# Kernel tuning notes

Measured on AMD Instinct MI355X. Metric: run time of the kernel, lower is better.

The kernel has to match this reference:

```python
import jax, jax.numpy as jnp
import numpy as np

N = 32768      # nodes
E = 1048576    # edges (avg degree 32)
H = 64         # hidden dim
T = 5          # message-passing rounds

def _mlp(x, W1, b1, W2, b2):
    # two-layer MLP with ReLU, applied row-wise
    return jax.nn.relu(x @ W1 + b1) @ W2 + b2

def setup_inputs() -> dict:
    key = jax.random.key(0)
    ks = jax.random.split(key, 24)
    g = lambda i, shape: jax.random.normal(ks[i], shape, dtype=jnp.float32) * (1.0 / np.sqrt(shape[0]))
    inp = {
        "nodes": jax.random.normal(ks[0], (N,), dtype=jnp.float32),
        "edges_init": jax.random.normal(ks[1], (E,), dtype=jnp.float32),
        "receivers": jax.random.randint(ks[2], (E,), 0, N, dtype=jnp.int32),
        "senders": jax.random.randint(ks[3], (E,), 0, N, dtype=jnp.int32),
        # NodeEncoder: 1 -> H -> H
        "Wne1": g(4, (1, H)), "bne1": jnp.zeros((H,), jnp.float32),
        "Wne2": g(5, (H, H)), "bne2": jnp.zeros((H,), jnp.float32),
        # EdgeEncoder: 1 -> H -> H
        "Wee1": g(6, (1, H)), "bee1": jnp.zeros((H,), jnp.float32),
        "Wee2": g(7, (H, H)), "bee2": jnp.zeros((H,), jnp.float32),
        # MessagePass edge-update MLP: [e, n_s, n_r] (3H) -> H -> H
        "Weu1": g(8, (3 * H, H)), "beu1": jnp.zeros((H,), jnp.float32),
        "Weu2": g(9, (H, H)), "beu2": jnp.zeros((H,), jnp.float32),
        # MessagePass node-update MLP: [n, agg] (2H) -> H -> H
        "Wnu1": g(10, (2 * H, H)), "bnu1": jnp.zeros((H,), jnp.float32),
        "Wnu2": g(11, (H, H)), "bnu2": jnp.zeros((H,), jnp.float32),
        # EdgeDecoder: H -> H -> 1
        "Wd1": g(12, (H, H)), "bd1": jnp.zeros((H,), jnp.float32),
        "Wd2": g(13, (H, 1)), "bd2": jnp.zeros((1,), jnp.float32),
        "alpha": jnp.float32(0.1),
    }
    return inp

def reference(nodes, edges_init, receivers, senders,
              Wne1, bne1, Wne2, bne2,
              Wee1, bee1, Wee2, bee2,
              Weu1, beu1, Weu2, beu2,
              Wnu1, bnu1, Wnu2, bnu2,
              Wd1, bd1, Wd2, bd2, alpha):
    norm = jnp.abs(edges_init).max()
    e = (edges_init / norm)[:, None]                   # [E,1]
    n = _mlp(nodes[:, None], Wne1, bne1, Wne2, bne2)   # [N,H]
    e = _mlp(e, Wee1, bee1, Wee2, bee2)                # [E,H]
    for _ in range(T):
        m = jnp.concatenate([e, n[senders], n[receivers]], axis=-1)  # [E,3H]
        e = _mlp(m, Weu1, beu1, Weu2, beu2)                          # [E,H]
        agg = jax.ops.segment_sum(e, receivers, num_segments=N)     # [N,H]
        n = _mlp(jnp.concatenate([n, agg], axis=-1), Wnu1, bnu1, Wnu2, bnu2)
    d = _mlp(e, Wd1, bd1, Wd2, bd2)[:, 0]              # [E]
    edges = edges_init + alpha * (d * norm)
    # graph_tril: keep lower-triangular entries (row=receiver >= col=sender);
    # sparse lower-tri matrix = BCOO((edges, [receivers, senders])); we return its values.
    edges = jnp.where(receivers >= senders, edges, jnp.float32(0.0))
    return edges
```

## Files before the change

kernel.cpp:

```cpp
#include <hip/hip_runtime.h>

#define NN 32768
#define NE 1048576
#define BCAP 5120

typedef __bf16 bf16_t;
typedef __bf16 bf16x8 __attribute__((ext_vector_type(8)));
typedef __bf16 bf16x4 __attribute__((ext_vector_type(4)));
typedef float f32x4 __attribute__((ext_vector_type(4)));
typedef unsigned int u32;
typedef unsigned short u16;

__global__ __launch_bounds__(256) void prep_encode_kernel(
    const float* __restrict__ Weu1, const float* __restrict__ Weu2,
    const float* __restrict__ Wee2, const float* __restrict__ Wd1,
    const float* __restrict__ Wnu1, const float* __restrict__ Wnu2,
    bf16_t* __restrict__ wfr,
    const float* __restrict__ nodes, const float* __restrict__ Wne1,
    const float* __restrict__ bne1, const float* __restrict__ Wne2,
    const float* __restrict__ bne2, bf16_t* __restrict__ n_bf) {
  const int b = blockIdx.x, tid = threadIdx.x;
  if (b < 144) {
    int idx = b * 256 + tid;
    int i = idx & 7, lane = (idx >> 3) & 63, f = idx >> 9;
    const float* W;
    int fl;
    if (f < 24)      { W = Weu1; fl = f; }
    else if (f < 32) { W = Weu2; fl = f - 24; }
    else if (f < 40) { W = Wee2; fl = f - 32; }
    else if (f < 48) { W = Wd1;  fl = f - 40; }
    else if (f < 64) { W = Wnu1; fl = f - 48; }
    else             { W = Wnu2; fl = f - 64; }
    int kt = fl >> 2, nt = fl & 3;
    int k = kt * 32 + ((lane >> 4) << 3) + i;
    int col = nt * 16 + (lane & 15);
    wfr[idx] = (bf16_t)W[k * 64 + col];
  } else {
    __shared__ float hs[4][64];
    int wid = tid >> 6, k = tid & 63;
    int node = (b - 144) * 4 + wid;
    float x = nodes[node];
    hs[wid][k] = fmaxf(x * Wne1[k] + bne1[k], 0.0f);
    __syncthreads();
    float acc = bne2[k];
#pragma unroll 8
    for (int j = 0; j < 64; ++j) acc = fmaf(hs[wid][j], Wne2[j * 64 + k], acc);
    n_bf[(size_t)node * 64 + k] = (bf16_t)acc;
  }
}

__global__ __launch_bounds__(256) void coarse_kernel(
    const float* __restrict__ edges_init, const int* __restrict__ recv,
    float* __restrict__ norm, u32* __restrict__ ccur,
    u16* __restrict__ bkt_r, u32* __restrict__ bkt_o) {
  __shared__ u32 hist[256];
  __shared__ u32 base[256];
  __shared__ float mred[4];
  const int tid = threadIdx.x, lane = tid & 63, wid = tid >> 6;
  const int idx = blockIdx.x * 256 + tid;
  hist[tid] = 0;
  __syncthreads();
  int4 r = reinterpret_cast<const int4*>(recv)[idx];
  float4 v = reinterpret_cast<const float4*>(edges_init)[idx];
  float m = fmaxf(fmaxf(fabsf(v.x), fabsf(v.y)), fmaxf(fabsf(v.z), fabsf(v.w)));
#pragma unroll
  for (int off = 32; off > 0; off >>= 1) m = fmaxf(m, __shfl_xor(m, off, 64));
  if (lane == 0) mred[wid] = m;
  atomicAdd(&hist[r.x >> 7], 1u);
  atomicAdd(&hist[r.y >> 7], 1u);
  atomicAdd(&hist[r.z >> 7], 1u);
  atomicAdd(&hist[r.w >> 7], 1u);
  __syncthreads();
  if (tid == 0) {
    float mm = fmaxf(fmaxf(mred[0], mred[1]), fmaxf(mred[2], mred[3]));
    atomicMax(reinterpret_cast<u32*>(norm), __float_as_uint(mm));
  }
  u32 h = hist[tid];
  if (h) base[tid] = atomicAdd(&ccur[tid], h);
  hist[tid] = 0;
  __syncthreads();
  const int e0 = idx * 4;
  int rv4[4] = {r.x, r.y, r.z, r.w};
#pragma unroll
  for (int q = 0; q < 4; ++q) {
    int rv = rv4[q], bk = rv >> 7;
    u32 loc = atomicAdd(&hist[bk], 1u);
    u32 pos = (u32)bk * BCAP + base[bk] + loc;
    bkt_r[pos] = (u16)rv;
    bkt_o[pos] = (u32)(e0 + q);
  }
}

__global__ __launch_bounds__(256) void scan256_kernel(const u32* __restrict__ ccur,
                                                      u32* __restrict__ bbase,
                                                      int* __restrict__ row_ptr) {
  __shared__ u32 s[256];
  const int tid = threadIdx.x;
  s[tid] = ccur[tid];
  __syncthreads();
  if (tid == 0) {
    u32 run = 0;
    for (int j = 0; j < 256; ++j) {
      u32 c = s[j];
      s[j] = run;
      run += c;
    }
    row_ptr[NN] = (int)run;
  }
  __syncthreads();
  bbase[tid] = s[tid];
}

__global__ __launch_bounds__(1024) void bucket_kernel(
    const u32* __restrict__ ccur, const u32* __restrict__ bbase,
    const u16* __restrict__ bkt_r, const u32* __restrict__ bkt_o,
    const int* __restrict__ senders, const float* __restrict__ edges_init,
    int* __restrict__ row_ptr, int* __restrict__ col_idx,
    int* __restrict__ s_perm, int* __restrict__ r_perm, float* __restrict__ x_perm) {
  __shared__ u32 hist[128];
  __shared__ u32 cur[128];
  const int b = blockIdx.x, tid = threadIdx.x;
  const u32 sz = ccur[b], bb = bbase[b];
  if (tid < 128) hist[tid] = 0;
  __syncthreads();
  for (u32 i = tid; i < sz; i += 1024) atomicAdd(&hist[bkt_r[(u32)b * BCAP + i] & 127], 1u);
  __syncthreads();
  if (tid == 0) {
    u32 run = 0;
    for (int j = 0; j < 128; ++j) {
      u32 c = hist[j];
      hist[j] = run;
      cur[j] = run;
      run += c;
    }
  }
  __syncthreads();
  if (tid < 128) row_ptr[b * 128 + tid] = (int)(bb + hist[tid]);
  for (u32 i = tid; i < sz; i += 1024) {
    int rv = (int)bkt_r[(u32)b * BCAP + i];
    int o = (int)bkt_o[(u32)b * BCAP + i];
    u32 loc = atomicAdd(&cur[rv & 127], 1u);
    u32 pos = bb + loc;
    col_idx[pos] = o;
    s_perm[pos] = senders[o];
    r_perm[pos] = rv;
    x_perm[pos] = edges_init[o];
  }
}

template <int MODE>
__global__ __launch_bounds__(256) void edge_update_kernel(
    bf16_t* __restrict__ e, const bf16_t* __restrict__ n_bf,
    const int* __restrict__ col_idx,
    const int* __restrict__ s_perm, const int* __restrict__ r_perm,
    const float* __restrict__ x_perm,
    const bf16_t* __restrict__ wfr,
    const float* __restrict__ beu1, const float* __restrict__ beu2,
    const float* __restrict__ Wee1, const float* __restrict__ bee1,
    const float* __restrict__ bee2, const float* __restrict__ norm_p,
    const float* __restrict__ bd1, const float* __restrict__ Wd2,
    const float* __restrict__ bd2_p, const float* __restrict__ alpha_p,
    float* __restrict__ out) {
  __shared__ alignas(16) bf16_t wstage[40 * 512];
  __shared__ alignas(16) bf16_t tr[4][16][72];
  __shared__ alignas(16) float fconst[448];
  const int tid = threadIdx.x, lane = tid & 63, wid = tid >> 6;
  const int l15 = lane & 15, lg = lane >> 4;

#pragma unroll
  for (int j = 0; j < 10; ++j) {
    int c = j * 256 + tid;
    int slot = c >> 6, within = c & 63;
    int sf = (slot < 32) ? slot : (MODE == 2 ? slot + 8 : slot);
    *reinterpret_cast<bf16x8*>(wstage + slot * 512 + within * 8) =
        *reinterpret_cast<const bf16x8*>(wfr + (size_t)sf * 512 + within * 8);
  }
  for (int c = tid; c < 448; c += 256) {
    float v;
    if (c < 64)       v = Wee1[c];
    else if (c < 128) v = bee1[c - 64];
    else if (c < 192) v = bee2[c - 128];
    else if (c < 256) v = bd1[c - 192];
    else if (c < 320) v = Wd2[c - 256];
    else if (c < 384) v = beu1[c - 320];
    else              v = beu2[c - 384];
    fconst[c] = v;
  }
  __syncthreads();

  float invn = 0.f;
  if constexpr (MODE == 0) invn = 1.0f / *norm_p;
  float nrm = 0.f, alp = 0.f, b2s = 0.f;
  if constexpr (MODE == 2) { nrm = *norm_p; alp = *alpha_p; b2s = *bd2_p; }

  const int nb = gridDim.x, cpx = nb >> 3;
  const int bs = (blockIdx.x & 7) * cpx + (blockIdx.x >> 3);
  const int NWAVE = nb * 4;
  const int NG = NE / 16;
  const int g0 = bs * 4 + wid;

  int sA, rA, oA, sB, rB, oB, sC, rC, oC;
  float pxA = 0.f, pxB = 0.f, pxC = 0.f;
  bf16x8 eA0, eA1, eB0, eB1, eC0, eC1;
  bf16x8 nA0, nA1, nA2, nA3, nB0, nB1, nB2, nB3;

  auto P1 = [&](int g, int& s, int& r, int& o, float& px, bf16x8& e0, bf16x8& e1) {
    int row = g * 16 + l15;
    s = s_perm[row];
    r = r_perm[row];
    if constexpr (MODE != 1) px = x_perm[row];
    if constexpr (MODE == 2) o = col_idx[row];
    if constexpr (MODE != 0) {
      const bf16x8* er = reinterpret_cast<const bf16x8*>(e + (size_t)row * 64);
      e0 = er[lg];
      e1 = er[4 + lg];
    }
  };
  auto P2 = [&](int s, int r, bf16x8& n0, bf16x8& n1, bf16x8& n2, bf16x8& n3) {
    const bf16x8* sp = reinterpret_cast<const bf16x8*>(n_bf + (size_t)s * 64);
    n0 = sp[lg];
    n1 = sp[4 + lg];
    const bf16x8* rp = reinterpret_cast<const bf16x8*>(n_bf + (size_t)r * 64);
    n2 = rp[lg];
    n3 = rp[4 + lg];
  };

  if (g0 < NG) {
    P1(g0, sA, rA, oA, pxA, eA0, eA1);
    P2(sA, rA, nA0, nA1, nA2, nA3);
    int g1 = g0 + NWAVE;
    if (g1 < NG) P1(g1, sB, rB, oB, pxB, eB0, eB1);
  }

  for (int g = g0; g < NG; g += NWAVE) {
    const int gB = g + NWAVE, gC = g + 2 * NWAVE;
    if (gB < NG) P2(sB, rB, nB0, nB1, nB2, nB3);
    if (gC < NG) P1(gC, sC, rC, oC, pxC, eC0, eC1);

    bf16x8 ce0, ce1;
    if constexpr (MODE == 0) {
      float xv = pxA * invn;
      f32x4 wl0 = *reinterpret_cast<const f32x4*>(&fconst[lg * 8]);
      f32x4 wl1 = *reinterpret_cast<const f32x4*>(&fconst[lg * 8 + 4]);
      f32x4 wh0 = *reinterpret_cast<const f32x4*>(&fconst[32 + lg * 8]);
      f32x4 wh1 = *reinterpret_cast<const f32x4*>(&fconst[32 + lg * 8 + 4]);
      f32x4 bl0 = *reinterpret_cast<const f32x4*>(&fconst[64 + lg * 8]);
      f32x4 bl1 = *reinterpret_cast<const f32x4*>(&fconst[64 + lg * 8 + 4]);
      f32x4 bh0 = *reinterpret_cast<const f32x4*>(&fconst[96 + lg * 8]);
      f32x4 bh1 = *reinterpret_cast<const f32x4*>(&fconst[96 + lg * 8 + 4]);
      bf16x8 h0, h1;
#pragma unroll
      for (int i = 0; i < 4; ++i) {
        h0[i]     = (bf16_t)fmaxf(fmaf(xv, wl0[i], bl0[i]), 0.0f);
        h0[4 + i] = (bf16_t)fmaxf(fmaf(xv, wl1[i], bl1[i]), 0.0f);
        h1[i]     = (bf16_t)fmaxf(fmaf(xv, wh0[i], bh0[i]), 0.0f);
        h1[4 + i] = (bf16_t)fmaxf(fmaf(xv, wh1[i], bh1[i]), 0.0f);
      }
      f32x4 ae[4];
#pragma unroll
      for (int nt = 0; nt < 4; ++nt)
        ae[nt] = *reinterpret_cast<const f32x4*>(&fconst[128 + nt * 16 + lg * 4]);
#pragma unroll
      for (int kt = 0; kt < 2; ++kt)
#pragma unroll
        for (int nt = 0; nt < 4; ++nt) {
          bf16x8 wf = *reinterpret_cast<const bf16x8*>(wstage + (32 + kt * 4 + nt) * 512 + lane * 8);
          ae[nt] = __builtin_amdgcn_mfma_f32_16x16x32_bf16(wf, kt ? h1 : h0, ae[nt], 0, 0, 0);
        }
#pragma unroll
      for (int nt = 0; nt < 4; ++nt) {
        bf16x4 pk;
#pragma unroll
        for (int r = 0; r < 4; ++r) pk[r] = (bf16_t)ae[nt][r];
        *reinterpret_cast<bf16x4*>(&tr[wid][l15][nt * 16 + lg * 4]) = pk;
      }
      ce0 = *reinterpret_cast<const bf16x8*>(&tr[wid][l15][lg * 8]);
      ce1 = *reinterpret_cast<const bf16x8*>(&tr[wid][l15][32 + lg * 8]);
    } else {
      ce0 = eA0;
      ce1 = eA1;
    }

    f32x4 acc[4];
#pragma unroll
    for (int nt = 0; nt < 4; ++nt)
      acc[nt] = *reinterpret_cast<const f32x4*>(&fconst[320 + nt * 16 + lg * 4]);
#pragma unroll
    for (int kt = 0; kt < 6; ++kt) {
      bf16x8 m = (kt == 0) ? ce0 : (kt == 1) ? ce1 : (kt == 2) ? nA0
               : (kt == 3) ? nA1 : (kt == 4) ? nA2 : nA3;
#pragma unroll
      for (int nt = 0; nt < 4; ++nt) {
        bf16x8 w = *reinterpret_cast<const bf16x8*>(wstage + (kt * 4 + nt) * 512 + lane * 8);
        acc[nt] = __builtin_amdgcn_mfma_f32_16x16x32_bf16(w, m, acc[nt], 0, 0, 0);
      }
    }

#pragma unroll
    for (int nt = 0; nt < 4; ++nt) {
      bf16x4 pk;
#pragma unroll
      for (int r = 0; r < 4; ++r) pk[r] = (bf16_t)fmaxf(acc[nt][r], 0.0f);
      *reinterpret_cast<bf16x4*>(&tr[wid][l15][nt * 16 + lg * 4]) = pk;
    }
    bf16x8 hh0 = *reinterpret_cast<const bf16x8*>(&tr[wid][l15][lg * 8]);
    bf16x8 hh1 = *reinterpret_cast<const bf16x8*>(&tr[wid][l15][32 + lg * 8]);

    f32x4 acc2[4];
#pragma unroll
    for (int nt = 0; nt < 4; ++nt)
      acc2[nt] = *reinterpret_cast<const f32x4*>(&fconst[384 + nt * 16 + lg * 4]);
#pragma unroll
    for (int kt = 0; kt < 2; ++kt)
#pragma unroll
      for (int nt = 0; nt < 4; ++nt) {
        bf16x8 w = *reinterpret_cast<const bf16x8*>(wstage + (24 + kt * 4 + nt) * 512 + lane * 8);
        acc2[nt] = __builtin_amdgcn_mfma_f32_16x16x32_bf16(w, kt ? hh1 : hh0, acc2[nt], 0, 0, 0);
      }

    if constexpr (MODE == 2) {
#pragma unroll
      for (int nt = 0; nt < 4; ++nt) {
        bf16x4 pk;
#pragma unroll
        for (int r = 0; r < 4; ++r) pk[r] = (bf16_t)acc2[nt][r];
        *reinterpret_cast<bf16x4*>(&tr[wid][l15][nt * 16 + lg * 4]) = pk;
      }
      bf16x8 eb0 = *reinterpret_cast<const bf16x8*>(&tr[wid][l15][lg * 8]);
      bf16x8 eb1 = *reinterpret_cast<const bf16x8*>(&tr[wid][l15][32 + lg * 8]);
      f32x4 ad[4];
#pragma unroll
      for (int nt = 0; nt < 4; ++nt)
        ad[nt] = *reinterpret_cast<const f32x4*>(&fconst[192 + nt * 16 + lg * 4]);
#pragma unroll
      for (int kt = 0; kt < 2; ++kt)
#pragma unroll
        for (int nt = 0; nt < 4; ++nt) {
          bf16x8 wf = *reinterpret_cast<const bf16x8*>(wstage + (32 + kt * 4 + nt) * 512 + lane * 8);
          ad[nt] = __builtin_amdgcn_mfma_f32_16x16x32_bf16(wf, kt ? eb1 : eb0, ad[nt], 0, 0, 0);
        }
      float s = 0.0f;
#pragma unroll
      for (int nt = 0; nt < 4; ++nt) {
        f32x4 w2 = *reinterpret_cast<const f32x4*>(&fconst[256 + nt * 16 + lg * 4]);
#pragma unroll
        for (int r = 0; r < 4; ++r) s = fmaf(fmaxf(ad[nt][r], 0.0f), w2[r], s);
      }
      s += __shfl_xor(s, 16, 64);
      s += __shfl_xor(s, 32, 64);
      if (lg == 0) {
        float dv = s + b2s;
        out[oA] = (rA >= sA) ? fmaf(alp * nrm, dv, pxA) : 0.0f;
      }
    } else {
#pragma unroll
      for (int nt = 0; nt < 4; ++nt) {
        bf16x4 pk;
#pragma unroll
        for (int r = 0; r < 4; ++r) pk[r] = (bf16_t)acc2[nt][r];
        *reinterpret_cast<bf16x4*>(&tr[wid][l15][nt * 16 + lg * 4]) = pk;
      }
      const int rr = lane >> 3, cc = lane & 7;
      bf16x8 w0 = *reinterpret_cast<const bf16x8*>(&tr[wid][rr][cc * 8]);
      bf16x8 w1 = *reinterpret_cast<const bf16x8*>(&tr[wid][8 + rr][cc * 8]);
      *reinterpret_cast<bf16x8*>(e + (size_t)(g * 16 + rr) * 64 + cc * 8) = w0;
      *reinterpret_cast<bf16x8*>(e + (size_t)(g * 16 + 8 + rr) * 64 + cc * 8) = w1;
    }

    sA = sB; rA = rB; oA = oB; pxA = pxB;
    eA0 = eB0; eA1 = eB1;
    nA0 = nB0; nA1 = nB1; nA2 = nB2; nA3 = nB3;
    sB = sC; rB = rC; oB = oC; pxB = pxC;
    eB0 = eC0; eB1 = eC1;
  }
}

__global__ __launch_bounds__(256) void agg_kernel(const bf16_t* __restrict__ e,
                                                  const int* __restrict__ row_ptr,
                                                  bf16_t* __restrict__ agg) {
  const int lane = threadIdx.x & 63, wid = threadIdx.x >> 6;
  const int rsub = lane >> 3;
  const int gw = blockIdx.x * 4 + wid, NWV = gridDim.x * 4;
  for (int node = gw; node < NN; node += NWV) {
    const int p0 = row_ptr[node], cnt = row_ptr[node + 1] - p0;
    float a[8] = {0, 0, 0, 0, 0, 0, 0, 0};
    const bf16x8* bb = reinterpret_cast<const bf16x8*>(e + (size_t)p0 * 64) + lane;
    const int nchunk = (cnt + 7) >> 3;
    int c = 0;
    for (; c + 4 <= nchunk; c += 4) {
      bf16x8 v0 = bb[(size_t)(c + 0) * 64];
      bf16x8 v1 = bb[(size_t)(c + 1) * 64];
      bf16x8 v2 = bb[(size_t)(c + 2) * 64];
      bf16x8 v3 = bb[(size_t)(c + 3) * 64];
      {
#pragma unroll
        for (int i = 0; i < 8; ++i) a[i] += (float)v0[i];
#pragma unroll
        for (int i = 0; i < 8; ++i) a[i] += (float)v1[i];
#pragma unroll
        for (int i = 0; i < 8; ++i) a[i] += (float)v2[i];
      }
      if ((c + 3) * 8 + rsub < cnt) {
#pragma unroll
        for (int i = 0; i < 8; ++i) a[i] += (float)v3[i];
      }
    }
    for (; c < nchunk; ++c) {
      bf16x8 v = bb[(size_t)c * 64];
      if (c * 8 + rsub < cnt) {
#pragma unroll
        for (int i = 0; i < 8; ++i) a[i] += (float)v[i];
      }
    }
#pragma unroll
    for (int i = 0; i < 8; ++i) {
      a[i] += __shfl_xor(a[i], 8, 64);
      a[i] += __shfl_xor(a[i], 16, 64);
      a[i] += __shfl_xor(a[i], 32, 64);
    }
    if (lane < 8) {
      bf16x8 pk;
#pragma unroll
      for (int i = 0; i < 8; ++i) pk[i] = (bf16_t)a[i];
      *reinterpret_cast<bf16x8*>(agg + (size_t)node * 64 + lane * 8) = pk;
    }
  }
}

__global__ __launch_bounds__(256) void node_mlp_kernel(
    const bf16_t* __restrict__ agg, const bf16_t* __restrict__ wfr,
    const float* __restrict__ bnu1, const float* __restrict__ bnu2,
    bf16_t* __restrict__ n_bf) {
  __shared__ alignas(16) bf16_t w2s[8 * 512];
  __shared__ alignas(16) bf16_t xb[4][16][72];
  const int tid = threadIdx.x, lane = tid & 63, wid = tid >> 6;
  const int l15 = lane & 15, lg = lane >> 4;

  bf16x8 W1r[16];
#pragma unroll
  for (int f = 0; f < 16; ++f)
    W1r[f] = *reinterpret_cast<const bf16x8*>(wfr + (size_t)(48 + f) * 512 + lane * 8);
#pragma unroll
  for (int j = 0; j < 2; ++j)
    reinterpret_cast<bf16x8*>(w2s)[j * 256 + tid] =
        reinterpret_cast<const bf16x8*>(wfr + (size_t)64 * 512)[j * 256 + tid];
  __syncthreads();

  f32x4 b1q[4], b2q[4];
#pragma unroll
  for (int nt = 0; nt < 4; ++nt) {
    b1q[nt] = *reinterpret_cast<const f32x4*>(bnu1 + nt * 16 + lg * 4);
    b2q[nt] = *reinterpret_cast<const f32x4*>(bnu2 + nt * 16 + lg * 4);
  }

  const int NT = NN / 16;
  for (int task = blockIdx.x * 4 + wid; task < NT; task += gridDim.x * 4) {
    const int base = task * 16;
    bf16x8 xn0 = *reinterpret_cast<const bf16x8*>(n_bf + (size_t)(base + l15) * 64 + lg * 8);
    bf16x8 xn1 = *reinterpret_cast<const bf16x8*>(n_bf + (size_t)(base + l15) * 64 + 32 + lg * 8);
    bf16x8 xa0 = *reinterpret_cast<const bf16x8*>(agg + (size_t)(base + l15) * 64 + lg * 8);
    bf16x8 xa1 = *reinterpret_cast<const bf16x8*>(agg + (size_t)(base + l15) * 64 + 32 + lg * 8);
    f32x4 acc[4];
#pragma unroll
    for (int nt = 0; nt < 4; ++nt) acc[nt] = b1q[nt];
#pragma unroll
    for (int kt = 0; kt < 4; ++kt) {
      bf16x8 x = (kt == 0) ? xn0 : (kt == 1) ? xn1 : (kt == 2) ? xa0 : xa1;
#pragma unroll
      for (int nt = 0; nt < 4; ++nt)
        acc[nt] = __builtin_amdgcn_mfma_f32_16x16x32_bf16(W1r[kt * 4 + nt], x, acc[nt], 0, 0, 0);
    }
#pragma unroll
    for (int nt = 0; nt < 4; ++nt) {
      bf16x4 pk;
#pragma unroll
      for (int r = 0; r < 4; ++r) pk[r] = (bf16_t)fmaxf(acc[nt][r], 0.0f);
      *reinterpret_cast<bf16x4*>(&xb[wid][l15][nt * 16 + lg * 4]) = pk;
    }
    bf16x8 hh0 = *reinterpret_cast<const bf16x8*>(&xb[wid][l15][lg * 8]);
    bf16x8 hh1 = *reinterpret_cast<const bf16x8*>(&xb[wid][l15][32 + lg * 8]);
    f32x4 acc2[4];
#pragma unroll
    for (int nt = 0; nt < 4; ++nt) acc2[nt] = b2q[nt];
#pragma unroll
    for (int kt = 0; kt < 2; ++kt)
#pragma unroll
      for (int nt = 0; nt < 4; ++nt) {
        bf16x8 w = *reinterpret_cast<const bf16x8*>(w2s + (kt * 4 + nt) * 512 + lane * 8);
        acc2[nt] = __builtin_amdgcn_mfma_f32_16x16x32_bf16(w, kt ? hh1 : hh0, acc2[nt], 0, 0, 0);
      }
#pragma unroll
    for (int nt = 0; nt < 4; ++nt) {
      bf16x4 pk;
#pragma unroll
      for (int r = 0; r < 4; ++r) pk[r] = (bf16_t)acc2[nt][r];
      *reinterpret_cast<bf16x4*>(n_bf + (size_t)(base + l15) * 64 + nt * 16 + lg * 4) = pk;
    }
  }
}

extern "C" void kernel_launch(void* const* d_in, const int* in_sizes, int n_in,
                              void* d_out, int out_size, void* d_ws, size_t ws_size,
                              hipStream_t stream) {
  const float* nodes      = (const float*)d_in[0];
  const float* edges_init = (const float*)d_in[1];
  const int*   receivers  = (const int*)d_in[2];
  const int*   senders    = (const int*)d_in[3];
  const float* Wne1 = (const float*)d_in[4];
  const float* bne1 = (const float*)d_in[5];
  const float* Wne2 = (const float*)d_in[6];
  const float* bne2 = (const float*)d_in[7];
  const float* Wee1 = (const float*)d_in[8];
  const float* bee1 = (const float*)d_in[9];
  const float* Wee2 = (const float*)d_in[10];
  const float* bee2 = (const float*)d_in[11];
  const float* Weu1 = (const float*)d_in[12];
  const float* beu1 = (const float*)d_in[13];
  const float* Weu2 = (const float*)d_in[14];
  const float* beu2 = (const float*)d_in[15];
  const float* Wnu1 = (const float*)d_in[16];
  const float* bnu1 = (const float*)d_in[17];
  const float* Wnu2 = (const float*)d_in[18];
  const float* bnu2 = (const float*)d_in[19];
  const float* Wd1  = (const float*)d_in[20];
  const float* bd1  = (const float*)d_in[21];
  const float* Wd2  = (const float*)d_in[22];
  const float* bd2  = (const float*)d_in[23];
  const float* alpha = (const float*)d_in[24];
  float* out = (float*)d_out;
  (void)in_sizes; (void)n_in; (void)out_size; (void)ws_size;

  char* ws = (char*)d_ws;
  size_t off = 0;
  auto alloc = [&](size_t bytes) -> void* {
    void* p = ws + off;
    off = (off + bytes + 255) & ~(size_t)255;
    return p;
  };
  float*  norm    = (float*)alloc(4);
  u32*    ccur    = (u32*)alloc(sizeof(u32) * 256);
  u32*    bbase   = (u32*)alloc(sizeof(u32) * 256);
  int*    row_ptr = (int*)alloc(sizeof(int) * (NN + 1));
  u16*    bkt_r   = (u16*)alloc(sizeof(u16) * 256 * BCAP);
  u32*    bkt_o   = (u32*)alloc(sizeof(u32) * 256 * BCAP);
  int*    col_idx = (int*)alloc(sizeof(int) * NE);
  int*    s_perm  = (int*)alloc(sizeof(int) * NE);
  int*    r_perm  = (int*)alloc(sizeof(int) * NE);
  float*  x_perm  = (float*)alloc(sizeof(float) * NE);
  bf16_t* n_bf    = (bf16_t*)alloc(sizeof(bf16_t) * (size_t)NN * 64);
  bf16_t* agg     = (bf16_t*)alloc(sizeof(bf16_t) * (size_t)NN * 64);
  bf16_t* e_buf   = (bf16_t*)alloc(sizeof(bf16_t) * (size_t)NE * 64 + 4096);
  bf16_t* wfr     = (bf16_t*)alloc(sizeof(bf16_t) * 72 * 512);

  hipMemsetAsync(norm, 0, 4, stream);
  hipMemsetAsync(ccur, 0, sizeof(u32) * 256, stream);

  prep_encode_kernel<<<8336, 256, 0, stream>>>(Weu1, Weu2, Wee2, Wd1, Wnu1, Wnu2, wfr,
                                               nodes, Wne1, bne1, Wne2, bne2, n_bf);
  coarse_kernel<<<1024, 256, 0, stream>>>(edges_init, receivers, norm, ccur, bkt_r, bkt_o);
  scan256_kernel<<<1, 256, 0, stream>>>(ccur, bbase, row_ptr);
  bucket_kernel<<<256, 1024, 0, stream>>>(ccur, bbase, bkt_r, bkt_o, senders, edges_init,
                                          row_ptr, col_idx, s_perm, r_perm, x_perm);

  edge_update_kernel<0><<<768, 256, 0, stream>>>(
      e_buf, n_bf, col_idx, s_perm, r_perm, x_perm, wfr, beu1, beu2,
      Wee1, bee1, bee2, norm, bd1, Wd2, bd2, alpha, out);
  for (int t = 1; t <= 4; ++t) {
    agg_kernel<<<2048, 256, 0, stream>>>(e_buf, row_ptr, agg);
    node_mlp_kernel<<<512, 256, 0, stream>>>(agg, wfr, bnu1, bnu2, n_bf);
    if (t < 4)
      edge_update_kernel<1><<<768, 256, 0, stream>>>(
          e_buf, n_bf, col_idx, s_perm, r_perm, x_perm, wfr, beu1, beu2,
          Wee1, bee1, bee2, norm, bd1, Wd2, bd2, alpha, out);
    else
      edge_update_kernel<2><<<768, 256, 0, stream>>>(
          e_buf, n_bf, col_idx, s_perm, r_perm, x_perm, wfr, beu1, beu2,
          Wee1, bee1, bee2, norm, bd1, Wd2, bd2, alpha, out);
  }
}
```

Baseline: 606.2 us.

## Fuse segment aggregation with node MLP and raise priority around MFMA loops

Merges agg_kernel and node_mlp_kernel into one kernel. Each block aggregates 16 nodes into shared memory, then a single wave runs the two-layer node MLP on them. This removes one launch per round and the global agg buffer round trip. In exchange, three of four waves idle during the MLP, and every block reloads the weights into registers and LDS. It also wraps the MFMA loops in the edge update kernel with s_setprio so those waves get issue priority.

```diff
diff --git a/kernel.cpp b/kernel.cpp
--- a/kernel.cpp
+++ b/kernel.cpp
@@ -260,6 +260,7 @@
 #pragma unroll
       for (int nt = 0; nt < 4; ++nt)
         ae[nt] = *reinterpret_cast<const f32x4*>(&fconst[128 + nt * 16 + lg * 4]);
+      __builtin_amdgcn_s_setprio(1);
 #pragma unroll
       for (int kt = 0; kt < 2; ++kt)
 #pragma unroll
@@ -267,6 +268,7 @@
           bf16x8 wf = *reinterpret_cast<const bf16x8*>(wstage + (32 + kt * 4 + nt) * 512 + lane * 8);
           ae[nt] = __builtin_amdgcn_mfma_f32_16x16x32_bf16(wf, kt ? h1 : h0, ae[nt], 0, 0, 0);
         }
+      __builtin_amdgcn_s_setprio(0);
 #pragma unroll
       for (int nt = 0; nt < 4; ++nt) {
         bf16x4 pk;
@@ -285,6 +287,7 @@
 #pragma unroll
     for (int nt = 0; nt < 4; ++nt)
       acc[nt] = *reinterpret_cast<const f32x4*>(&fconst[320 + nt * 16 + lg * 4]);
+    __builtin_amdgcn_s_setprio(1);
 #pragma unroll
     for (int kt = 0; kt < 6; ++kt) {
       bf16x8 m = (kt == 0) ? ce0 : (kt == 1) ? ce1 : (kt == 2) ? nA0
@@ -295,6 +298,7 @@
         acc[nt] = __builtin_amdgcn_mfma_f32_16x16x32_bf16(w, m, acc[nt], 0, 0, 0);
       }
     }
+    __builtin_amdgcn_s_setprio(0);
 
 #pragma unroll
     for (int nt = 0; nt < 4; ++nt) {
@@ -310,6 +314,7 @@
 #pragma unroll
     for (int nt = 0; nt < 4; ++nt)
       acc2[nt] = *reinterpret_cast<const f32x4*>(&fconst[384 + nt * 16 + lg * 4]);
+    __builtin_amdgcn_s_setprio(1);
 #pragma unroll
     for (int kt = 0; kt < 2; ++kt)
 #pragma unroll
@@ -317,6 +322,7 @@
         bf16x8 w = *reinterpret_cast<const bf16x8*>(wstage + (24 + kt * 4 + nt) * 512 + lane * 8);
         acc2[nt] = __builtin_amdgcn_mfma_f32_16x16x32_bf16(w, kt ? hh1 : hh0, acc2[nt], 0, 0, 0);
       }
+    __builtin_amdgcn_s_setprio(0);
 
     if constexpr (MODE == 2) {
 #pragma unroll
@@ -332,6 +338,7 @@
 #pragma unroll
       for (int nt = 0; nt < 4; ++nt)
         ad[nt] = *reinterpret_cast<const f32x4*>(&fconst[192 + nt * 16 + lg * 4]);
+      __builtin_amdgcn_s_setprio(1);
 #pragma unroll
       for (int kt = 0; kt < 2; ++kt)
 #pragma unroll
@@ -339,6 +346,7 @@
           bf16x8 wf = *reinterpret_cast<const bf16x8*>(wstage + (32 + kt * 4 + nt) * 512 + lane * 8);
           ad[nt] = __builtin_amdgcn_mfma_f32_16x16x32_bf16(wf, kt ? eb1 : eb0, ad[nt], 0, 0, 0);
         }
+      __builtin_amdgcn_s_setprio(0);
       float s = 0.0f;
 #pragma unroll
       for (int nt = 0; nt < 4; ++nt) {
@@ -375,13 +383,29 @@
   }
 }
 
-__global__ __launch_bounds__(256) void agg_kernel(const bf16_t* __restrict__ e,
-                                                  const int* __restrict__ row_ptr,
-                                                  bf16_t* __restrict__ agg) {
-  const int lane = threadIdx.x & 63, wid = threadIdx.x >> 6;
+__global__ __launch_bounds__(256) void agg_mlp_kernel(
+    const bf16_t* __restrict__ e, const int* __restrict__ row_ptr,
+    const bf16_t* __restrict__ wfr,
+    const float* __restrict__ bnu1, const float* __restrict__ bnu2,
+    bf16_t* __restrict__ n_bf) {
+  __shared__ alignas(16) bf16_t w2s[8 * 512];
+  __shared__ alignas(16) bf16_t xb[16][72];
+  const int tid = threadIdx.x, lane = tid & 63, wid = tid >> 6;
+  const int l15 = lane & 15, lg = lane >> 4;
+  const int base = blockIdx.x * 16;
+
+  bf16x8 W1r[16];
+#pragma unroll
+  for (int f = 0; f < 16; ++f)
+    W1r[f] = *reinterpret_cast<const bf16x8*>(wfr + (size_t)(48 + f) * 512 + lane * 8);
+#pragma unroll
+  for (int j = 0; j < 2; ++j)
+    reinterpret_cast<bf16x8*>(w2s)[j * 256 + tid] =
+        reinterpret_cast<const bf16x8*>(wfr + (size_t)64 * 512)[j * 256 + tid];
+
   const int rsub = lane >> 3;
-  const int gw = blockIdx.x * 4 + wid, NWV = gridDim.x * 4;
-  for (int node = gw; node < NN; node += NWV) {
+  for (int j = 0; j < 4; ++j) {
+    const int node = base + wid * 4 + j;
     const int p0 = row_ptr[node], cnt = row_ptr[node + 1] - p0;
     float a[8] = {0, 0, 0, 0, 0, 0, 0, 0};
     const bf16x8* bb = reinterpret_cast<const bf16x8*>(e + (size_t)p0 * 64) + lane;
@@ -422,29 +446,11 @@
       bf16x8 pk;
 #pragma unroll
       for (int i = 0; i < 8; ++i) pk[i] = (bf16_t)a[i];
-      *reinterpret_cast<bf16x8*>(agg + (size_t)node * 64 + lane * 8) = pk;
-    }
-  }
-}
-
-__global__ __launch_bounds__(256) void node_mlp_kernel(
-    const bf16_t* __restrict__ agg, const bf16_t* __restrict__ wfr,
-    const float* __restrict__ bnu1, const float* __restrict__ bnu2,
-    bf16_t* __restrict__ n_bf) {
-  __shared__ alignas(16) bf16_t w2s[8 * 512];
-  __shared__ alignas(16) bf16_t xb[4][16][72];
-  const int tid = threadIdx.x, lane = tid & 63, wid = tid >> 6;
-  const int l15 = lane & 15, lg = lane >> 4;
-
-  bf16x8 W1r[16];
-#pragma unroll
-  for (int f = 0; f < 16; ++f)
-    W1r[f] = *reinterpret_cast<const bf16x8*>(wfr + (size_t)(48 + f) * 512 + lane * 8);
-#pragma unroll
-  for (int j = 0; j < 2; ++j)
-    reinterpret_cast<bf16x8*>(w2s)[j * 256 + tid] =
-        reinterpret_cast<const bf16x8*>(wfr + (size_t)64 * 512)[j * 256 + tid];
-  __syncthreads();
+      *reinterpret_cast<bf16x8*>(&xb[wid * 4 + j][lane * 8]) = pk;
+    }
+  }
+  __syncthreads();
+  if (wid != 0) return;
 
   f32x4 b1q[4], b2q[4];
 #pragma unroll
@@ -452,50 +458,45 @@
     b1q[nt] = *reinterpret_cast<const f32x4*>(bnu1 + nt * 16 + lg * 4);
     b2q[nt] = *reinterpret_cast<const f32x4*>(bnu2 + nt * 16 + lg * 4);
   }
-
-  const int NT = NN / 16;
-  for (int task = blockIdx.x * 4 + wid; task < NT; task += gridDim.x * 4) {
-    const int base = task * 16;
-    bf16x8 xn0 = *reinterpret_cast<const bf16x8*>(n_bf + (size_t)(base + l15) * 64 + lg * 8);
-    bf16x8 xn1 = *reinterpret_cast<const bf16x8*>(n_bf + (size_t)(base + l15) * 64 + 32 + lg * 8);
-    bf16x8 xa0 = *reinterpret_cast<const bf16x8*>(agg + (size_t)(base + l15) * 64 + lg * 8);
-    bf16x8 xa1 = *reinterpret_cast<const bf16x8*>(agg + (size_t)(base + l15) * 64 + 32 + lg * 8);
-    f32x4 acc[4];
-#pragma unroll
-    for (int nt = 0; nt < 4; ++nt) acc[nt] = b1q[nt];
-#pragma unroll
-    for (int kt = 0; kt < 4; ++kt) {
-      bf16x8 x = (kt == 0) ? xn0 : (kt == 1) ? xn1 : (kt == 2) ? xa0 : xa1;
-#pragma unroll
-      for (int nt = 0; nt < 4; ++nt)
-        acc[nt] = __builtin_amdgcn_mfma_f32_16x16x32_bf16(W1r[kt * 4 + nt], x, acc[nt], 0, 0, 0);
-    }
+  bf16x8 xn0 = *reinterpret_cast<const bf16x8*>(n_bf + (size_t)(base + l15) * 64 + lg * 8);
+  bf16x8 xn1 = *reinterpret_cast<const bf16x8*>(n_bf + (size_t)(base + l15) * 64 + 32 + lg * 8);
+  bf16x8 xa0 = *reinterpret_cast<const bf16x8*>(&xb[l15][lg * 8]);
+  bf16x8 xa1 = *reinterpret_cast<const bf16x8*>(&xb[l15][32 + lg * 8]);
+  f32x4 acc[4];
+#pragma unroll
+  for (int nt = 0; nt < 4; ++nt) acc[nt] = b1q[nt];
+#pragma unroll
+  for (int kt = 0; kt < 4; ++kt) {
+    bf16x8 x = (kt == 0) ? xn0 : (kt == 1) ? xn1 : (kt == 2) ? xa0 : xa1;
+#pragma unroll
+    for (int nt = 0; nt < 4; ++nt)
+      acc[nt] = __builtin_amdgcn_mfma_f32_16x16x32_bf16(W1r[kt * 4 + nt], x, acc[nt], 0, 0, 0);
+  }
+#pragma unroll
+  for (int nt = 0; nt < 4; ++nt) {
+    bf16x4 pk;
+#pragma unroll
+    for (int r = 0; r < 4; ++r) pk[r] = (bf16_t)fmaxf(acc[nt][r], 0.0f);
+    *reinterpret_cast<bf16x4*>(&xb[l15][nt * 16 + lg * 4]) = pk;
+  }
+  bf16x8 hh0 = *reinterpret_cast<const bf16x8*>(&xb[l15][lg * 8]);
+  bf16x8 hh1 = *reinterpret_cast<const bf16x8*>(&xb[l15][32 + lg * 8]);
+  f32x4 acc2[4];
+#pragma unroll
+  for (int nt = 0; nt < 4; ++nt) acc2[nt] = b2q[nt];
+#pragma unroll
+  for (int kt = 0; kt < 2; ++kt)
 #pragma unroll
     for (int nt = 0; nt < 4; ++nt) {
-      bf16x4 pk;
-#pragma unroll
-      for (int r = 0; r < 4; ++r) pk[r] = (bf16_t)fmaxf(acc[nt][r], 0.0f);
-      *reinterpret_cast<bf16x4*>(&xb[wid][l15][nt * 16 + lg * 4]) = pk;
-    }
-    bf16x8 hh0 = *reinterpret_cast<const bf16x8*>(&xb[wid][l15][lg * 8]);
-    bf16x8 hh1 = *reinterpret_cast<const bf16x8*>(&xb[wid][l15][32 + lg * 8]);
-    f32x4 acc2[4];
-#pragma unroll
-    for (int nt = 0; nt < 4; ++nt) acc2[nt] = b2q[nt];
-#pragma unroll
-    for (int kt = 0; kt < 2; ++kt)
-#pragma unroll
-      for (int nt = 0; nt < 4; ++nt) {
-        bf16x8 w = *reinterpret_cast<const bf16x8*>(w2s + (kt * 4 + nt) * 512 + lane * 8);
-        acc2[nt] = __builtin_amdgcn_mfma_f32_16x16x32_bf16(w, kt ? hh1 : hh0, acc2[nt], 0, 0, 0);
-      }
-#pragma unroll
-    for (int nt = 0; nt < 4; ++nt) {
-      bf16x4 pk;
-#pragma unroll
-      for (int r = 0; r < 4; ++r) pk[r] = (bf16_t)acc2[nt][r];
-      *reinterpret_cast<bf16x4*>(n_bf + (size_t)(base + l15) * 64 + nt * 16 + lg * 4) = pk;
-    }
+      bf16x8 w = *reinterpret_cast<const bf16x8*>(w2s + (kt * 4 + nt) * 512 + lane * 8);
+      acc2[nt] = __builtin_amdgcn_mfma_f32_16x16x32_bf16(w, kt ? hh1 : hh0, acc2[nt], 0, 0, 0);
+    }
+#pragma unroll
+  for (int nt = 0; nt < 4; ++nt) {
+    bf16x4 pk;
+#pragma unroll
+    for (int r = 0; r < 4; ++r) pk[r] = (bf16_t)acc2[nt][r];
+    *reinterpret_cast<bf16x4*>(n_bf + (size_t)(base + l15) * 64 + nt * 16 + lg * 4) = pk;
   }
 }
 
@@ -548,7 +549,6 @@
   int*    r_perm  = (int*)alloc(sizeof(int) * NE);
   float*  x_perm  = (float*)alloc(sizeof(float) * NE);
   bf16_t* n_bf    = (bf16_t*)alloc(sizeof(bf16_t) * (size_t)NN * 64);
-  bf16_t* agg     = (bf16_t*)alloc(sizeof(bf16_t) * (size_t)NN * 64);
   bf16_t* e_buf   = (bf16_t*)alloc(sizeof(bf16_t) * (size_t)NE * 64 + 4096);
   bf16_t* wfr     = (bf16_t*)alloc(sizeof(bf16_t) * 72 * 512);
 
@@ -566,8 +566,7 @@
       e_buf, n_bf, col_idx, s_perm, r_perm, x_perm, wfr, beu1, beu2,
       Wee1, bee1, bee2, norm, bd1, Wd2, bd2, alpha, out);
   for (int t = 1; t <= 4; ++t) {
-    agg_kernel<<<2048, 256, 0, stream>>>(e_buf, row_ptr, agg);
-    node_mlp_kernel<<<512, 256, 0, stream>>>(agg, wfr, bnu1, bnu2, n_bf);
+    agg_mlp_kernel<<<2048, 256, 0, stream>>>(e_buf, row_ptr, wfr, bnu1, bnu2, n_bf);
     if (t < 4)
       edge_update_kernel<1><<<768, 256, 0, stream>>>(
           e_buf, n_bf, col_idx, s_perm, r_perm, x_perm, wfr, beu1, beu2,
```

Measured after the change: 538.8 us. 11.1% less time.
